# Optimization experiments

Measured on AMD Instinct MI355X. Metric: run time of the kernel, lower is better.

Reference implementation:

```python
import jax, jax.numpy as jnp
import numpy as np

DIM_MODEL = 1024
DIM_K = 1024
DIM_V = 1024


def setup_inputs() -> dict:
    key = jax.random.key(0)
    ks = jax.random.split(key, 7)
    B, S = 4, 2048
    scale = 1.0 / np.sqrt(DIM_MODEL)
    return {
        "x": jax.random.normal(ks[0], (B, S, DIM_MODEL), dtype=jnp.float32),
        # weights stored [in, out] (transpose of torch Linear.weight)
        "Wq": jax.random.normal(ks[1], (DIM_MODEL, DIM_K), dtype=jnp.float32) * scale,
        "Wk": jax.random.normal(ks[2], (DIM_MODEL, DIM_K), dtype=jnp.float32) * scale,
        "Wv": jax.random.normal(ks[3], (DIM_MODEL, DIM_V), dtype=jnp.float32) * scale,
        "Wo": jax.random.normal(ks[4], (DIM_V, DIM_MODEL), dtype=jnp.float32) * (1.0 / np.sqrt(DIM_V)),
        "ln2_gamma": jnp.ones((DIM_MODEL,), dtype=jnp.float32),
        "ln2_beta": jnp.zeros((DIM_MODEL,), dtype=jnp.float32),
    }


def _layernorm(x, gamma, beta, eps=1e-5):
    mu = jnp.mean(x, axis=-1, keepdims=True)
    var = jnp.var(x, axis=-1, keepdims=True)
    return (x - mu) * jax.lax.rsqrt(var + eps) * gamma + beta


def reference(x, Wq, Wk, Wv, Wo, ln2_gamma, ln2_beta):
    # single-head attention, x: [B,S,D]
    q = jnp.einsum("bsd,dk->bsk", x, Wq)
    k = jnp.einsum("bsd,dk->bsk", x, Wk)
    v = jnp.einsum("bsd,dv->bsv", x, Wv)
    scores = jnp.einsum("bqk,bsk->bqs", q, k) / jnp.sqrt(jnp.asarray(DIM_K, x.dtype))
    attn = jax.nn.softmax(scores, axis=-1)  # [B,S,S]
    ctx = jnp.einsum("bqs,bsv->bqv", attn, v)
    hidden = jnp.einsum("bqv,vd->bqd", ctx, Wo)
    hidden = _layernorm(hidden, ln2_gamma, ln2_beta)
    return hidden
```

## Files before the change

### kernel.cpp

```cpp
#include <hip/hip_runtime.h>
#include <hip/hip_bf16.h>
#include <stdint.h>

typedef __bf16 bf16;
typedef __attribute__((ext_vector_type(8))) __bf16 bf16x8;
typedef __attribute__((ext_vector_type(4))) __bf16 bf16x4;
typedef __attribute__((ext_vector_type(4))) float f32x4;

#define AS1 __attribute__((address_space(1)))
#define AS3 __attribute__((address_space(3)))

__device__ __forceinline__ void gl_lds16(const void* g, void* l) {
  __builtin_amdgcn_global_load_lds((const AS1 uint32_t*)g, (AS3 uint32_t*)l, 16, 0, 0);
}

#define FENCE() asm volatile("" ::: "memory")
#define BAR()                        \
  do {                               \
    FENCE();                         \
    __builtin_amdgcn_s_barrier();    \
    FENCE();                         \
  } while (0)
#define VMW4() asm volatile("s_waitcnt vmcnt(4)" ::: "memory")

template <int MODE>
__global__ __launch_bounds__(512, 2) void gemm256(
    const bf16* __restrict__ Abase, const bf16* __restrict__ Bbase,
    bf16* __restrict__ Cbase, int K, int lda, int ldb, int ldc,
    long long sA, long long sB, long long sC, float alpha,
    float* __restrict__ lsum, bf16* __restrict__ C2, bf16* __restrict__ C3) {
  extern __shared__ char smem[];
  const int z = blockIdx.z;
  const bf16* A = Abase + (long long)z * sA;
  const bf16* B = Bbase + (long long)z * sB;
  bf16* C = Cbase + (long long)z * sC;
  const int m0 = blockIdx.y * 256, n0 = blockIdx.x * 256;
  const int t = threadIdx.x;
  const int lane = t & 63;
  const int wid = t >> 6, wrow = wid >> 2, wcol = wid & 3;
  const int quad = lane >> 4, r = lane & 15;

  const int rowq = t >> 3;
  const int chunk = (t & 7) ^ (rowq & 7);
  const bf16* pA0 = A + (long long)(m0 + rowq) * lda + chunk * 8;
  const bf16* pB0 = B + (long long)(n0 + rowq) * ldb + chunk * 8;

  const int aoff = (wrow * 64 + r) * 128;
  const int boff = 32768 + (wcol * 32 + r) * 128;
  const int cs0 = ((quad) ^ (r & 7)) * 16;
  const int cs1 = ((4 + quad) ^ (r & 7)) * 16;

#define STAGE_A(HALF, KT, SB)                                                  \
  do {                                                                         \
    gl_lds16(pA0 + (long long)((HALF) * 128) * lda + (KT),                     \
             (SB) + (HALF) * 16384 + t * 16);                                  \
    gl_lds16(pA0 + (long long)((HALF) * 128 + 64) * lda + (KT),                \
             (SB) + (HALF) * 16384 + 8192 + t * 16);                           \
  } while (0)
#define STAGE_B(HALF, KT, SB)                                                  \
  do {                                                                         \
    gl_lds16(pB0 + (long long)((HALF) * 128) * ldb + (KT),                     \
             (SB) + 32768 + (HALF) * 16384 + t * 16);                          \
    gl_lds16(pB0 + (long long)((HALF) * 128 + 64) * ldb + (KT),                \
             (SB) + 32768 + (HALF) * 16384 + 8192 + t * 16);                   \
  } while (0)
#define READ_A(MH)                                                             \
  _Pragma("unroll") for (int mr = 0; mr < 4; ++mr) {                           \
    af[mr][0] = *(const bf16x8*)(Sc + (MH) * 16384 + aoff + mr * 2048 + cs0);  \
    af[mr][1] = *(const bf16x8*)(Sc + (MH) * 16384 + aoff + mr * 2048 + cs1);  \
  }
#define READ_B(NH)                                                             \
  _Pragma("unroll") for (int nr = 0; nr < 2; ++nr) {                           \
    bfr[NH][nr][0] =                                                           \
        *(const bf16x8*)(Sc + (NH) * 16384 + boff + nr * 2048 + cs0);          \
    bfr[NH][nr][1] =                                                           \
        *(const bf16x8*)(Sc + (NH) * 16384 + boff + nr * 2048 + cs1);          \
  }
#define MMA(MH, NH)                                                            \
  _Pragma("unroll") for (int mr = 0; mr < 4; ++mr)                             \
      _Pragma("unroll") for (int nr = 0; nr < 2; ++nr) {                       \
    acc[MH][NH][mr][nr] = __builtin_amdgcn_mfma_f32_16x16x32_bf16(             \
        af[mr][0], bfr[NH][nr][0], acc[MH][NH][mr][nr], 0, 0, 0);              \
    acc[MH][NH][mr][nr] = __builtin_amdgcn_mfma_f32_16x16x32_bf16(             \
        af[mr][1], bfr[NH][nr][1], acc[MH][NH][mr][nr], 0, 0, 0);              \
  }

  f32x4 acc[2][2][4][2] = {};
  bf16x8 af[4][2];
  bf16x8 bfr[2][2][2];
  char* Sc = smem;
  char* Sn = smem + 65536;
  const int T = K >> 6;

  STAGE_A(0, 0, Sc);
  STAGE_B(0, 0, Sc);
  STAGE_A(1, 0, Sc);
  STAGE_B(1, 0, Sc);
  {
    const int kt1p = (T > 1) ? 64 : 0;
    STAGE_A(0, kt1p, Sn);
    STAGE_B(0, kt1p, Sn);
  }
  VMW4();
  BAR();

  for (int tt = 0; tt < T; ++tt) {
    const int kt1 = (tt + 1 < T ? tt + 1 : 0) << 6;
    const int kt2 = (tt + 2 < T ? tt + 2 : 0) << 6;
    READ_A(0);
    READ_B(0);
    STAGE_A(1, kt1, Sn);
    __builtin_amdgcn_s_setprio(1);
    MMA(0, 0);
    __builtin_amdgcn_s_setprio(0);
    BAR();
    READ_B(1);
    STAGE_B(1, kt1, Sn);
    __builtin_amdgcn_s_setprio(1);
    MMA(0, 1);
    __builtin_amdgcn_s_setprio(0);
    BAR();
    READ_A(1);
    STAGE_A(0, kt2, Sc);
    __builtin_amdgcn_s_setprio(1);
    MMA(1, 0);
    __builtin_amdgcn_s_setprio(0);
    BAR();
    STAGE_B(0, kt2, Sc);
    __builtin_amdgcn_s_setprio(1);
    MMA(1, 1);
    __builtin_amdgcn_s_setprio(0);
    VMW4();
    BAR();
    char* tp = Sc;
    Sc = Sn;
    Sn = tp;
  }

  if constexpr (MODE == 4) {
    bf16* dst;
    int c0;
    if (n0 < 1024) {
      dst = Cbase;
      c0 = n0;
    } else if (n0 < 2048) {
      dst = C2;
      c0 = n0 - 1024;
    } else {
      dst = C3;
      c0 = n0 - 2048;
    }
#pragma unroll
    for (int mh = 0; mh < 2; ++mh)
#pragma unroll
      for (int mr = 0; mr < 4; ++mr) {
        const int row0 = m0 + mh * 128 + wrow * 64 + mr * 16 + quad * 4;
#pragma unroll
        for (int nh = 0; nh < 2; ++nh)
#pragma unroll
          for (int nr = 0; nr < 2; ++nr) {
            const int col = c0 + nh * 128 + wcol * 32 + nr * 16 + r;
#pragma unroll
            for (int rg = 0; rg < 4; ++rg)
              dst[(long long)(row0 + rg) * 1024 + col] =
                  (bf16)acc[mh][nh][mr][nr][rg];
          }
      }
    return;
  }

#pragma unroll
  for (int mh = 0; mh < 2; ++mh)
#pragma unroll
    for (int mr = 0; mr < 4; ++mr) {
      const int row0 = m0 + mh * 128 + wrow * 64 + mr * 16 + quad * 4;
      float rsum[4] = {0.f, 0.f, 0.f, 0.f};
      float inv[4];
      if constexpr (MODE == 2) {
#pragma unroll
        for (int rg = 0; rg < 4; ++rg)
          inv[rg] = 1.f / lsum[(long long)z * 2048 + row0 + rg];
      }
#pragma unroll
      for (int nh = 0; nh < 2; ++nh)
#pragma unroll
        for (int nr = 0; nr < 2; ++nr) {
          const int col = n0 + nh * 128 + wcol * 32 + nr * 16 + r;
#pragma unroll
          for (int rg = 0; rg < 4; ++rg) {
            float v = acc[mh][nh][mr][nr][rg] * alpha;
            if constexpr (MODE == 1) {
              bf16 eb = (bf16)__expf(v);
              C[(long long)(row0 + rg) * ldc + col] = eb;
              rsum[rg] += (float)eb;
            } else if constexpr (MODE == 2) {
              C[(long long)(row0 + rg) * ldc + col] = (bf16)(v * inv[rg]);
            } else {
              C[(long long)(row0 + rg) * ldc + col] = (bf16)v;
            }
          }
        }
      if constexpr (MODE == 1) {
#pragma unroll
        for (int rg = 0; rg < 4; ++rg) {
#pragma unroll
          for (int off = 8; off >= 1; off >>= 1)
            rsum[rg] += __shfl_xor(rsum[rg], off);
          if (r == 0)
            atomicAdd(&lsum[(long long)z * 2048 + row0 + rg], rsum[rg]);
        }
      }
    }
#undef STAGE_A
#undef STAGE_B
#undef READ_A
#undef READ_B
#undef MMA
}

template <int MODE>
__global__ __launch_bounds__(256, 3) void gemm128(
    const bf16* __restrict__ Abase, const bf16* __restrict__ Bbase,
    bf16* __restrict__ Cbase, int K, int lda, int ldb, int ldc,
    long long sA, long long sB, long long sC, float alpha,
    float* __restrict__ lsum, bf16* __restrict__ C2, bf16* __restrict__ C3) {
  extern __shared__ char smem[];
  const int z = blockIdx.z;
  const bf16* A = Abase + (long long)z * sA;
  const bf16* B = Bbase + (long long)z * sB;
  bf16* C = Cbase + (long long)z * sC;
  const int m0 = blockIdx.y * 128, n0 = blockIdx.x * 128;
  const int t = threadIdx.x;
  const int lane = t & 63, wave = t >> 6;
  const int wm = (wave >> 1) * 64, wn = (wave & 1) * 64;
  const int quad = lane >> 4, r = lane & 15;

  const int srow = t >> 3;
  const int schunk = (t & 7) ^ (srow & 7);
  const bf16* ga = A + (long long)(m0 + srow) * lda + schunk * 8;
  const bf16* gb = B + (long long)(n0 + srow) * ldb + schunk * 8;
  char* la = smem + t * 16;
  char* lb = smem + 16384 + t * 16;

  f32x4 acc[4][4] = {};

  for (int k0 = 0; k0 < K; k0 += 64) {
    __syncthreads();
#pragma unroll
    for (int rd = 0; rd < 4; rd++) {
      gl_lds16(ga + (long long)(32 * rd) * lda, la + rd * 4096);
      gl_lds16(gb + (long long)(32 * rd) * ldb, lb + rd * 4096);
    }
    ga += 64;
    gb += 64;
    __syncthreads();

#pragma unroll
    for (int kk = 0; kk < 2; kk++) {
      bf16x8 af[4], bfr[4];
      const int csa = ((kk * 4 + quad) ^ (r & 7)) * 16;
      const char* pa = smem + (wm + r) * 128 + csa;
      const char* pb = smem + 16384 + (wn + r) * 128 + csa;
#pragma unroll
      for (int i = 0; i < 4; i++) af[i] = *(const bf16x8*)(pa + i * 2048);
#pragma unroll
      for (int j = 0; j < 4; j++) bfr[j] = *(const bf16x8*)(pb + j * 2048);
#pragma unroll
      for (int i = 0; i < 4; i++)
#pragma unroll
        for (int j = 0; j < 4; j++)
          acc[i][j] = __builtin_amdgcn_mfma_f32_16x16x32_bf16(af[i], bfr[j],
                                                              acc[i][j], 0, 0, 0);
    }
  }

  if constexpr (MODE == 4) {
    bf16* dst;
    int c0;
    if (n0 < 1024) {
      dst = Cbase; c0 = n0;
    } else if (n0 < 2048) {
      dst = C2; c0 = n0 - 1024;
    } else {
      dst = C3; c0 = n0 - 2048;
    }
#pragma unroll
    for (int i = 0; i < 4; i++) {
      const int row0 = m0 + wm + i * 16 + quad * 4;
#pragma unroll
      for (int j = 0; j < 4; j++) {
        const int col = c0 + wn + j * 16 + r;
#pragma unroll
        for (int rg = 0; rg < 4; rg++)
          dst[(long long)(row0 + rg) * 1024 + col] = (bf16)acc[i][j][rg];
      }
    }
    return;
  }

#pragma unroll
  for (int i = 0; i < 4; i++) {
    const int row0 = m0 + wm + i * 16 + quad * 4;
    float rsum[4] = {0.f, 0.f, 0.f, 0.f};
    float inv[4];
    if constexpr (MODE == 2) {
#pragma unroll
      for (int rg = 0; rg < 4; rg++)
        inv[rg] = 1.f / lsum[(long long)z * 2048 + row0 + rg];
    }
#pragma unroll
    for (int j = 0; j < 4; j++) {
      const int col = n0 + wn + j * 16 + r;
#pragma unroll
      for (int rg = 0; rg < 4; rg++) {
        float v = acc[i][j][rg] * alpha;
        if constexpr (MODE == 1) {
          bf16 eb = (bf16)__expf(v);
          C[(long long)(row0 + rg) * ldc + col] = eb;
          rsum[rg] += (float)eb;
        } else if constexpr (MODE == 2) {
          C[(long long)(row0 + rg) * ldc + col] = (bf16)(v * inv[rg]);
        } else {
          C[(long long)(row0 + rg) * ldc + col] = (bf16)v;
        }
      }
    }
    if constexpr (MODE == 1) {
#pragma unroll
      for (int rg = 0; rg < 4; rg++) {
#pragma unroll
        for (int off = 8; off >= 1; off >>= 1)
          rsum[rg] += __shfl_xor(rsum[rg], off);
        if (r == 0)
          atomicAdd(&lsum[(long long)z * 2048 + row0 + rg], rsum[rg]);
      }
    }
  }
}

__global__ __launch_bounds__(256) void prep(
    const float* __restrict__ x, const float* __restrict__ Wq,
    const float* __restrict__ Wk, const float* __restrict__ Wv,
    const float* __restrict__ Wo, bf16* __restrict__ Xb,
    bf16* __restrict__ Wcat, bf16* __restrict__ Wot,
    float* __restrict__ lsum) {
  __shared__ float tile[32][33];
  const int bx = blockIdx.x;
  const int t = threadIdx.x;
  if (bx < 4096) {
    if (bx < 32) lsum[bx * 256 + t] = 0.f;
    long long i = (long long)bx * 256 + t;
    const float4* p = (const float4*)x;
    float4 a = p[i * 2], b = p[i * 2 + 1];
    bf16x8 o;
    o[0] = (bf16)a.x; o[1] = (bf16)a.y; o[2] = (bf16)a.z; o[3] = (bf16)a.w;
    o[4] = (bf16)b.x; o[5] = (bf16)b.y; o[6] = (bf16)b.z; o[7] = (bf16)b.w;
    ((bf16x8*)Xb)[i] = o;
  } else {
    int idx = bx - 4096;
    const int zw = idx >> 10;
    idx &= 1023;
    const int tiy = idx >> 5, tix = idx & 31;
    const float* W = (zw == 0) ? Wq : (zw == 1) ? Wk : (zw == 2) ? Wv : Wo;
    bf16* dst = (zw < 3) ? (Wcat + (long long)zw * 1024 * 1024) : Wot;
    const int bx0 = tix * 32, by0 = tiy * 32;
    const int ttx = t & 31, tty = t >> 5;
#pragma unroll
    for (int i = 0; i < 32; i += 8)
      tile[tty + i][ttx] = W[(long long)(by0 + tty + i) * 1024 + bx0 + ttx];
    __syncthreads();
#pragma unroll
    for (int i = 0; i < 32; i += 8)
      dst[(long long)(bx0 + tty + i) * 1024 + by0 + ttx] = (bf16)tile[ttx][tty + i];
  }
}

__global__ __launch_bounds__(256) void layernorm_rows(
    const bf16* __restrict__ H, const float* __restrict__ gamma,
    const float* __restrict__ beta, float* __restrict__ O) {
  const long long row = blockIdx.x;
  const bf16* h = H + row * 1024;
  float* o = O + row * 1024;
  const int t = threadIdx.x;
  const int lane = t & 63, wave = t >> 6;
  bf16x4 hv = ((const bf16x4*)h)[t];
  float v[4] = {(float)hv[0], (float)hv[1], (float)hv[2], (float)hv[3]};
  float s = v[0] + v[1] + v[2] + v[3];
  float ss = v[0] * v[0] + v[1] * v[1] + v[2] * v[2] + v[3] * v[3];
#pragma unroll
  for (int off = 32; off >= 1; off >>= 1) {
    s += __shfl_xor(s, off);
    ss += __shfl_xor(ss, off);
  }
  __shared__ float rs[4], rss[4];
  if (lane == 0) {
    rs[wave] = s;
    rss[wave] = ss;
  }
  __syncthreads();
  s = rs[0] + rs[1] + rs[2] + rs[3];
  ss = rss[0] + rss[1] + rss[2] + rss[3];
  const float mean = s * (1.f / 1024.f);
  const float var = ss * (1.f / 1024.f) - mean * mean;
  const float rstd = rsqrtf(var + 1e-5f);
  float4 g = ((const float4*)gamma)[t];
  float4 bb = ((const float4*)beta)[t];
  float4 rr;
  rr.x = (v[0] - mean) * rstd * g.x + bb.x;
  rr.y = (v[1] - mean) * rstd * g.y + bb.y;
  rr.z = (v[2] - mean) * rstd * g.z + bb.z;
  rr.w = (v[3] - mean) * rstd * g.w + bb.w;
  ((float4*)o)[t] = rr;
}

extern "C" void kernel_launch(void* const* d_in, const int* in_sizes, int n_in,
                              void* d_out, int out_size, void* d_ws,
                              size_t ws_size, hipStream_t stream) {
  const float* x = (const float*)d_in[0];
  const float* Wq = (const float*)d_in[1];
  const float* Wk = (const float*)d_in[2];
  const float* Wv = (const float*)d_in[3];
  const float* Wo = (const float*)d_in[4];
  const float* gamma = (const float*)d_in[5];
  const float* beta = (const float*)d_in[6];
  float* out = (float*)d_out;

  char* ws = (char*)d_ws;
  const size_t MB = 1024ull * 1024ull;
  bf16* Xb = (bf16*)(ws + 0);
  bf16* Wcat = (bf16*)(ws + 16 * MB);
  bf16* Wot = (bf16*)(ws + 22 * MB);
  bf16* Qd = (bf16*)(ws + 24 * MB);
  bf16* Kd = (bf16*)(ws + 40 * MB);
  bf16* Vd = (bf16*)(ws + 56 * MB);
  bf16* expS = (bf16*)(ws + 72 * MB);
  float* lsum = (float*)(ws + 104 * MB);
  bf16* VWo = (bf16*)(ws + 105 * MB);
  bf16* Hd = (bf16*)(ws + 121 * MB);

  static int inited = 0;
  if (!inited) {
    hipFuncSetAttribute(reinterpret_cast<const void*>(&gemm256<1>),
                        hipFuncAttributeMaxDynamicSharedMemorySize, 131072);
    inited = 1;
  }

  prep<<<8192, 256, 0, stream>>>(x, Wq, Wk, Wv, Wo, Xb, Wcat, Wot, lsum);

  gemm128<4><<<dim3(24, 64, 1), 256, 32768, stream>>>(
      Xb, Wcat, Qd, 1024, 1024, 1024, 1024, 0, 0, 0, 1.f, nullptr, Kd, Vd);

  gemm256<1><<<dim3(8, 8, 4), 512, 131072, stream>>>(
      Qd, Kd, expS, 1024, 1024, 1024, 2048, 2048 * 1024LL, 2048 * 1024LL,
      2048 * 2048LL, 0.03125f, lsum, nullptr, nullptr);

  gemm128<0><<<dim3(16, 8, 4), 256, 32768, stream>>>(
      Wot, Vd, VWo, 1024, 1024, 1024, 2048, 0, 2048 * 1024LL, 1024 * 2048LL,
      1.f, nullptr, nullptr, nullptr);

  gemm128<2><<<dim3(8, 16, 4), 256, 32768, stream>>>(
      expS, VWo, Hd, 2048, 2048, 2048, 1024, 2048 * 2048LL, 1024 * 2048LL,
      2048 * 1024LL, 1.f, lsum, nullptr, nullptr);

  layernorm_rows<<<8192, 256, 0, stream>>>(Hd, gamma, beta, out);
}
```

Measured before the change: 263.1 us.

## Overlap V·Wo GEMM on second stream and move softmax normalization into layernorm

Launches the V·Wo product on a separate non-blocking stream, synchronized with events, so it can run concurrently with the QK^T/exp GEMM. It also removes the per-row 1/lsum scaling from the final attention GEMM epilogue and applies it in the layernorm kernel instead, which lets gemm128 drop its MODE-specific epilogue code. The intent is to fill idle CUs during the score GEMM and to simplify the epilogue. The cost is stream and event overhead, plus possible contention between the two concurrent kernels. Storing unnormalized bf16 H before scaling may also slightly change precision.

```diff
diff --git a/kernel.cpp b/kernel.cpp
--- a/kernel.cpp
+++ b/kernel.cpp
@@ -175,12 +175,6 @@
     for (int mr = 0; mr < 4; ++mr) {
       const int row0 = m0 + mh * 128 + wrow * 64 + mr * 16 + quad * 4;
       float rsum[4] = {0.f, 0.f, 0.f, 0.f};
-      float inv[4];
-      if constexpr (MODE == 2) {
-#pragma unroll
-        for (int rg = 0; rg < 4; ++rg)
-          inv[rg] = 1.f / lsum[(long long)z * 2048 + row0 + rg];
-      }
 #pragma unroll
       for (int nh = 0; nh < 2; ++nh)
 #pragma unroll
@@ -193,8 +187,6 @@
               bf16 eb = (bf16)__expf(v);
               C[(long long)(row0 + rg) * ldc + col] = eb;
               rsum[rg] += (float)eb;
-            } else if constexpr (MODE == 2) {
-              C[(long long)(row0 + rg) * ldc + col] = (bf16)(v * inv[rg]);
             } else {
               C[(long long)(row0 + rg) * ldc + col] = (bf16)v;
             }
@@ -223,7 +215,7 @@
     const bf16* __restrict__ Abase, const bf16* __restrict__ Bbase,
     bf16* __restrict__ Cbase, int K, int lda, int ldb, int ldc,
     long long sA, long long sB, long long sC, float alpha,
-    float* __restrict__ lsum, bf16* __restrict__ C2, bf16* __restrict__ C3) {
+    bf16* __restrict__ C2, bf16* __restrict__ C3) {
   extern __shared__ char smem[];
   const int z = blockIdx.z;
   const bf16* A = Abase + (long long)z * sA;
@@ -301,38 +293,13 @@
 #pragma unroll
   for (int i = 0; i < 4; i++) {
     const int row0 = m0 + wm + i * 16 + quad * 4;
-    float rsum[4] = {0.f, 0.f, 0.f, 0.f};
-    float inv[4];
-    if constexpr (MODE == 2) {
-#pragma unroll
-      for (int rg = 0; rg < 4; rg++)
-        inv[rg] = 1.f / lsum[(long long)z * 2048 + row0 + rg];
-    }
 #pragma unroll
     for (int j = 0; j < 4; j++) {
       const int col = n0 + wn + j * 16 + r;
 #pragma unroll
       for (int rg = 0; rg < 4; rg++) {
         float v = acc[i][j][rg] * alpha;
-        if constexpr (MODE == 1) {
-          bf16 eb = (bf16)__expf(v);
-          C[(long long)(row0 + rg) * ldc + col] = eb;
-          rsum[rg] += (float)eb;
-        } else if constexpr (MODE == 2) {
-          C[(long long)(row0 + rg) * ldc + col] = (bf16)(v * inv[rg]);
-        } else {
-          C[(long long)(row0 + rg) * ldc + col] = (bf16)v;
-        }
-      }
-    }
-    if constexpr (MODE == 1) {
-#pragma unroll
-      for (int rg = 0; rg < 4; rg++) {
-#pragma unroll
-        for (int off = 8; off >= 1; off >>= 1)
-          rsum[rg] += __shfl_xor(rsum[rg], off);
-        if (r == 0)
-          atomicAdd(&lsum[(long long)z * 2048 + row0 + rg], rsum[rg]);
+        C[(long long)(row0 + rg) * ldc + col] = (bf16)v;
       }
     }
   }
@@ -376,15 +343,18 @@
 }
 
 __global__ __launch_bounds__(256) void layernorm_rows(
-    const bf16* __restrict__ H, const float* __restrict__ gamma,
-    const float* __restrict__ beta, float* __restrict__ O) {
+    const bf16* __restrict__ H, const float* __restrict__ lsum,
+    const float* __restrict__ gamma, const float* __restrict__ beta,
+    float* __restrict__ O) {
   const long long row = blockIdx.x;
   const bf16* h = H + row * 1024;
   float* o = O + row * 1024;
   const int t = threadIdx.x;
   const int lane = t & 63, wave = t >> 6;
+  const float invl = 1.f / lsum[row];
   bf16x4 hv = ((const bf16x4*)h)[t];
-  float v[4] = {(float)hv[0], (float)hv[1], (float)hv[2], (float)hv[3]};
+  float v[4] = {(float)hv[0] * invl, (float)hv[1] * invl, (float)hv[2] * invl,
+                (float)hv[3] * invl};
   float s = v[0] + v[1] + v[2] + v[3];
   float ss = v[0] * v[0] + v[1] * v[1] + v[2] * v[2] + v[3] * v[3];
 #pragma unroll
@@ -438,29 +408,38 @@
   bf16* VWo = (bf16*)(ws + 105 * MB);
   bf16* Hd = (bf16*)(ws + 121 * MB);
 
-  static int inited = 0;
-  if (!inited) {
+  static hipStream_t s2 = nullptr;
+  static hipEvent_t evA = nullptr, evB = nullptr;
+  if (!s2) {
+    hipStreamCreateWithFlags(&s2, hipStreamNonBlocking);
+    hipEventCreateWithFlags(&evA, hipEventDisableTiming);
+    hipEventCreateWithFlags(&evB, hipEventDisableTiming);
     hipFuncSetAttribute(reinterpret_cast<const void*>(&gemm256<1>),
                         hipFuncAttributeMaxDynamicSharedMemorySize, 131072);
-    inited = 1;
   }
 
   prep<<<8192, 256, 0, stream>>>(x, Wq, Wk, Wv, Wo, Xb, Wcat, Wot, lsum);
 
   gemm128<4><<<dim3(24, 64, 1), 256, 32768, stream>>>(
-      Xb, Wcat, Qd, 1024, 1024, 1024, 1024, 0, 0, 0, 1.f, nullptr, Kd, Vd);
+      Xb, Wcat, Qd, 1024, 1024, 1024, 1024, 0, 0, 0, 1.f, Kd, Vd);
+
+  hipEventRecord(evA, stream);
+  hipStreamWaitEvent(s2, evA, 0);
+
+  gemm128<0><<<dim3(16, 8, 4), 256, 32768, s2>>>(
+      Wot, Vd, VWo, 1024, 1024, 1024, 2048, 0, 2048 * 1024LL, 1024 * 2048LL,
+      1.f, nullptr, nullptr);
+  hipEventRecord(evB, s2);
 
   gemm256<1><<<dim3(8, 8, 4), 512, 131072, stream>>>(
       Qd, Kd, expS, 1024, 1024, 1024, 2048, 2048 * 1024LL, 2048 * 1024LL,
       2048 * 2048LL, 0.03125f, lsum, nullptr, nullptr);
 
-  gemm128<0><<<dim3(16, 8, 4), 256, 32768, stream>>>(
-      Wot, Vd, VWo, 1024, 1024, 1024, 2048, 0, 2048 * 1024LL, 1024 * 2048LL,
-      1.f, nullptr, nullptr, nullptr);
-
-  gemm128<2><<<dim3(8, 16, 4), 256, 32768, stream>>>(
+  hipStreamWaitEvent(stream, evB, 0);
+
+  gemm128<0><<<dim3(8, 16, 4), 256, 32768, stream>>>(
       expS, VWo, Hd, 2048, 2048, 2048, 1024, 2048 * 2048LL, 1024 * 2048LL,
-      2048 * 1024LL, 1.f, lsum, nullptr, nullptr);
-
-  layernorm_rows<<<8192, 256, 0, stream>>>(Hd, gamma, beta, out);
-}
+      2048 * 1024LL, 1.f, nullptr, nullptr);
+
+  layernorm_rows<<<8192, 256, 0, stream>>>(Hd, lsum, gamma, beta, out);
+}
```

After: 273.3 us. 3.9% more time.
